# Optimization experiments

Hardware: AMD Instinct MI355X
Metric: run time of the kernel (lower is better)

## Reference

```python
import jax, jax.numpy as jnp
import numpy as np

SKIP = 2 ** -0.5
EPS = 1e-6
DIM = 1024
N_LAYERS = 8
N_HEADS = 16
MAX_SEQ = 1024
B = 4
L = 1024


def get_rot_emb(dim, max_seq_len):
    pos = jnp.arange(max_seq_len, dtype=jnp.float32)
    omega = 1.0 / 10000.0 ** (jnp.arange(0, dim, 2, dtype=jnp.float32) / dim)
    angles = pos[:, None] * omega[None, :]  # [S, dim/2]
    cos = jnp.repeat(jnp.cos(angles), 2, axis=-1)  # [S, dim]
    sin = jnp.repeat(jnp.sin(angles), 2, axis=-1)
    return cos, sin


def setup_inputs() -> dict:
    key = jax.random.key(0)
    ks = jax.random.split(key, 16)
    s = 0.02
    d = DIM
    nl = N_LAYERS
    cos, sin = get_rot_emb(d // N_HEADS, MAX_SEQ)
    inp = {
        'x': jax.random.normal(ks[0], (B, L, d), jnp.float32),
        'c': jax.random.normal(ks[1], (B, 1, d), jnp.float32),
        't': jax.random.normal(ks[2], (B, d), jnp.float32),
        'num_heads': N_HEADS,
        'cos': cos,
        'sin': sin,
        'qkv_w': jax.random.normal(ks[3], (nl, d, 3 * d), jnp.float32) * s,
        'qkv_b': jnp.zeros((nl, 3 * d), jnp.float32),
        'proj_w': jax.random.normal(ks[4], (nl, d, d), jnp.float32) * s,
        'proj_b': jnp.zeros((nl, d), jnp.float32),
        'mlp_w1': jax.random.normal(ks[5], (nl, d, 4 * d), jnp.float32) * s,
        'mlp_b1': jnp.zeros((nl, 4 * d), jnp.float32),
        'mlp_w2': jax.random.normal(ks[6], (nl, 4 * d, d), jnp.float32) * s,
        'mlp_b2': jnp.zeros((nl, d), jnp.float32),
        'adaln_w': jax.random.normal(ks[7], (nl, d, 6 * d), jnp.float32) * s,
        'adaln_b': jnp.zeros((nl, 6 * d), jnp.float32),
    }
    return inp


def layer_norm(x):
    mu = jnp.mean(x, axis=-1, keepdims=True)
    var = jnp.var(x, axis=-1, keepdims=True)
    return (x - mu) * jax.lax.rsqrt(var + EPS)


def rotate_half(q):
    # torch: stack([-q[..., 1::2], q[..., ::2]], -1).reshape(q.shape)
    q2 = q.reshape(q.shape[:-1] + (-1, 2))
    return jnp.stack([-q2[..., 1], q2[..., 0]], axis=-1).reshape(q.shape)


def reference(x, c, t, num_heads, cos, sin, qkv_w, qkv_b, proj_w, proj_b, mlp_w1, mlp_b1, mlp_w2, mlp_b2, adaln_w, adaln_b):
    Bx, Lx, C = x.shape
    H = int(num_heads)
    D = C // H
    scale = D ** -0.5
    cmod = (c + t[:, None]) * SKIP  # [B,1,C]
    cos_l = cos[:Lx]  # [L,D]
    sin_l = sin[:Lx]

    def block(xcur, p):
        qw, qb, pw, pb, w1, b1, w2, b2, aw, ab = p
        mod = jax.nn.silu(cmod) @ aw + ab  # [B,1,6C]
        sh1, sc1, g1, sh2, sc2, g2 = jnp.split(mod, 6, axis=-1)
        h = (layer_norm(xcur) * (1 + sc1) + sh1) * SKIP
        qkv = (h @ qw + qb).reshape(Bx, Lx, 3, H, D).transpose(2, 0, 3, 1, 4)
        q, k, v = qkv[0], qkv[1], qkv[2]  # [B,H,L,D]
        q = q * cos_l + rotate_half(q) * sin_l
        k = k * cos_l + rotate_half(k) * sin_l
        attn = jax.nn.softmax(scale * jnp.einsum('bhid,bhjd->bhij', q, k), axis=-1)
        o = jnp.einsum('bhij,bhjd->bhid', attn, v).transpose(0, 2, 1, 3).reshape(Bx, Lx, C)
        o = o @ pw + pb
        xcur = (xcur + g1 * o) * SKIP
        h2 = (layer_norm(xcur) * (1 + sc2) + sh2) * SKIP
        m = jax.nn.gelu(h2 @ w1 + b1, approximate=True) @ w2 + b2
        return (xcur + g2 * m) * SKIP, None

    params = (qkv_w, qkv_b, proj_w, proj_b, mlp_w1, mlp_b1, mlp_w2, mlp_b2, adaln_w, adaln_b)
    out, _ = jax.lax.scan(block, x, params)
    return out
```

## Files before the change

kernel.cpp:

```cpp
#include <hip/hip_runtime.h>

#define SKIPF 0.70710678118654752440f

typedef unsigned short u16;
typedef unsigned int u32;
typedef __attribute__((ext_vector_type(4))) short bf16x4;
typedef __attribute__((ext_vector_type(8))) short bf16x8;
typedef __attribute__((ext_vector_type(4))) float f32x4;

#define MFMA32(A, B, C) __builtin_amdgcn_mfma_f32_16x16x32_bf16(A, B, C, 0, 0, 0)
#define MFMA16(A, B, C) __builtin_amdgcn_mfma_f32_16x16x16bf16_1k(A, B, C, 0, 0, 0)

__device__ __forceinline__ float bf2f(u16 v) {
  u32 u = ((u32)v) << 16; float f; __builtin_memcpy(&f, &u, 4); return f;
}
__device__ __forceinline__ u16 f2bf(float f) {
  u32 u; __builtin_memcpy(&u, &f, 4);
  u = (u + 0x7fffu + ((u >> 16) & 1u)) >> 16;
  return (u16)u;
}
__device__ __forceinline__ u32 cvtpk(float a, float b) {
  u32 r;
  asm("v_cvt_pk_bf16_f32 %0, %1, %2" : "=v"(r) : "v"(a), "v"(b));
  return r;
}
__device__ __forceinline__ void gload16(const void* g, void* s) {
  __builtin_amdgcn_global_load_lds((const __attribute__((address_space(1))) void*)g,
                                   (__attribute__((address_space(3))) void*)s, 16, 0, 0);
}

__global__ __launch_bounds__(256) void adaln_part_kernel(const float* __restrict__ c,
                                                         const float* __restrict__ t,
                                                         const float* __restrict__ aw,
                                                         float* __restrict__ part) {
  __shared__ float sc[4][32];
  int n = blockIdx.x * 256 + threadIdx.x;
  int ks = blockIdx.y;
  int k0 = ks * 32;
  if (threadIdx.x < 128) {
    int b = threadIdx.x >> 5, kk = threadIdx.x & 31;
    float xx = (c[b * 1024 + k0 + kk] + t[b * 1024 + k0 + kk]) * SKIPF;
    sc[b][kk] = xx / (1.f + __expf(-xx));
  }
  __syncthreads();
  float a0 = 0.f, a1 = 0.f, a2 = 0.f, a3 = 0.f;
#pragma unroll 4
  for (int k = 0; k < 32; ++k) {
    float w = aw[(size_t)(k0 + k) * 6144 + n];
    a0 += sc[0][k] * w; a1 += sc[1][k] * w; a2 += sc[2][k] * w; a3 += sc[3][k] * w;
  }
  part[(size_t)(ks * 4 + 0) * 6144 + n] = a0;
  part[(size_t)(ks * 4 + 1) * 6144 + n] = a1;
  part[(size_t)(ks * 4 + 2) * 6144 + n] = a2;
  part[(size_t)(ks * 4 + 3) * 6144 + n] = a3;
}

__global__ void adaln_reduce_kernel(const float* __restrict__ part, const float* __restrict__ ab,
                                    float* __restrict__ mod) {
  int i = blockIdx.x * 256 + threadIdx.x;
  int b = i / 6144, n = i - b * 6144;
  float a = ab[n];
#pragma unroll 4
  for (int ks = 0; ks < 32; ++ks) a += part[(size_t)(ks * 4 + b) * 6144 + n];
  mod[(size_t)b * 6144 + n] = a;
}

__global__ void wtrans4_kernel(const float* __restrict__ wq, u16* __restrict__ oq,
                               const float* __restrict__ wp, u16* __restrict__ op,
                               const float* __restrict__ w1p, u16* __restrict__ o1,
                               const float* __restrict__ w2p, u16* __restrict__ o2) {
  __shared__ float tile[32][33];
  int bid = blockIdx.x;
  const float* W; u16* WT; int nx, K, N, base;
  if (bid < 3072)      { W = wq;  WT = oq; nx = 96;  K = 1024; N = 3072; base = 0; }
  else if (bid < 4096) { W = wp;  WT = op; nx = 32;  K = 1024; N = 1024; base = 3072; }
  else if (bid < 8192) { W = w1p; WT = o1; nx = 128; K = 1024; N = 4096; base = 4096; }
  else                 { W = w2p; WT = o2; nx = 32;  K = 4096; N = 1024; base = 8192; }
  int t = bid - base;
  int n0 = (t % nx) * 32, k0 = (t / nx) * 32;
  int tx = threadIdx.x, ty = threadIdx.y;
#pragma unroll
  for (int i = 0; i < 4; ++i)
    tile[ty * 4 + i][tx] = W[(size_t)(k0 + ty * 4 + i) * N + n0 + tx];
  __syncthreads();
#pragma unroll
  for (int i = 0; i < 4; ++i)
    WT[(size_t)(n0 + ty * 4 + i) * K + k0 + tx] = f2bf(tile[tx][ty * 4 + i]);
}

__global__ __launch_bounds__(256) void ln_mod_kernel(const float* __restrict__ xin,
                                                     const float* __restrict__ mod,
                                                     u16* __restrict__ h, int sh_off, int sc_off) {
  int row = blockIdx.x;
  int b = row >> 10;
  const float4* xr = (const float4*)(xin + (size_t)row * 1024);
  float4 v = xr[threadIdx.x];
  float s = v.x + v.y + v.z + v.w;
  float ss = v.x * v.x + v.y * v.y + v.z * v.z + v.w * v.w;
#pragma unroll
  for (int o = 32; o; o >>= 1) { s += __shfl_xor(s, o); ss += __shfl_xor(ss, o); }
  __shared__ float red[8];
  int wave = threadIdx.x >> 6;
  if ((threadIdx.x & 63) == 0) { red[wave * 2] = s; red[wave * 2 + 1] = ss; }
  __syncthreads();
  s = red[0] + red[2] + red[4] + red[6];
  ss = red[1] + red[3] + red[5] + red[7];
  float mu = s * (1.f / 1024.f);
  float var = ss * (1.f / 1024.f) - mu * mu;
  float rs = rsqrtf(var + 1e-6f);
  int n = threadIdx.x * 4;
  const float* mb = mod + (size_t)b * 6144;
  float4 sc = *(const float4*)(mb + sc_off + n);
  float4 sh = *(const float4*)(mb + sh_off + n);
  ushort4 o4;
  o4.x = f2bf(((v.x - mu) * rs * (1.f + sc.x) + sh.x) * SKIPF);
  o4.y = f2bf(((v.y - mu) * rs * (1.f + sc.y) + sh.y) * SKIPF);
  o4.z = f2bf(((v.z - mu) * rs * (1.f + sc.z) + sh.z) * SKIPF);
  o4.w = f2bf(((v.w - mu) * rs * (1.f + sc.w) + sh.w) * SKIPF);
  *(ushort4*)(h + (size_t)row * 1024 + n) = o4;
}

template <int EPI>
__global__ __launch_bounds__(512, 1) void gemm256r_kernel(
    const u16* __restrict__ A, const u16* __restrict__ BT, const float* __restrict__ bias,
    u16* __restrict__ Cb, int NBX, int N, int K,
    const float* __restrict__ cosb, const float* __restrict__ sinb,
    u16* __restrict__ qo, u16* __restrict__ ko, u16* __restrict__ vto) {
  __shared__ u16 lds[4][16384];
  const int tid = threadIdx.x;
  const int lane = tid & 63, wave = tid >> 6;
  const int lq = lane & 15, lk = lane >> 4;
  const int wr = wave >> 2, wc = wave & 3;

  int per = gridDim.x >> 3;
  int swz = (blockIdx.x & 7) * per + (blockIdx.x >> 3);
  int bx = swz % NBX, by = swz / NBX;
  const int m0 = by * 256, n0 = bx * 256;

  f32x4 acc[8][4];
#pragma unroll
  for (int i = 0; i < 8; ++i)
#pragma unroll
    for (int j = 0; j < 4; ++j) acc[i][j] = (f32x4){0.f, 0.f, 0.f, 0.f};

  auto STAGE_ONE = [&](int slot, int t, int part) {
    int kt = t * 32;
    int u = tid + (part & 1) * 512;
    int r = u >> 3, cpos = u & 7;
    int g = cpos ^ (r & 7);
    if (part < 2) {
      gload16(A + (size_t)(m0 + 2 * r + (g >> 2)) * K + kt + (g & 3) * 8,
              (char*)lds[slot] + u * 16);
    } else {
      gload16(BT + (size_t)(n0 + 2 * r + (g >> 2)) * K + kt + (g & 3) * 8,
              (char*)(lds[slot] + 8192) + u * 16);
    }
  };
  auto STAGE = [&](int slot, int t) {
#pragma unroll
    for (int p = 0; p < 4; ++p) STAGE_ONE(slot, t, p);
  };

  const int NT = K >> 5;
  STAGE(0, 0); STAGE(1, 1); STAGE(2, 2);
  int slot = 0;
  for (int t = 0; t < NT; ++t) {
    int rem = NT - 1 - t;
    if (rem >= 2) asm volatile("s_waitcnt vmcnt(8)" ::: "memory");
    else if (rem == 1) asm volatile("s_waitcnt vmcnt(4)" ::: "memory");
    else asm volatile("s_waitcnt vmcnt(0)" ::: "memory");
    __builtin_amdgcn_s_barrier();
    __builtin_amdgcn_sched_barrier(0);
    const char* Ab = (const char*)lds[slot];
    const char* Bb = (const char*)(lds[slot] + 8192);
    int ns = slot + 3; if (ns >= 4) ns -= 4;
    bool pre = (t + 3 < NT);
    bf16x8 bfr[4];
#pragma unroll
    for (int ni = 0; ni < 4; ++ni) {
      int nrow = wc * 64 + ni * 16 + lq;
      int r = nrow >> 1, g = (nrow & 1) * 4 + lk;
      bfr[ni] = *(const bf16x8*)(Bb + r * 128 + ((g ^ (r & 7)) << 4));
    }
#pragma unroll
    for (int ph = 0; ph < 4; ++ph) {
      if (pre) STAGE_ONE(ns, t + 3, ph);
      bf16x8 af0, af1;
      {
        int mrow = wr * 128 + (ph * 2) * 16 + lq;
        int r = mrow >> 1, g = (mrow & 1) * 4 + lk;
        af0 = *(const bf16x8*)(Ab + r * 128 + ((g ^ (r & 7)) << 4));
        mrow += 16;
        r = mrow >> 1; g = (mrow & 1) * 4 + lk;
        af1 = *(const bf16x8*)(Ab + r * 128 + ((g ^ (r & 7)) << 4));
      }
      __builtin_amdgcn_s_setprio(1);
#pragma unroll
      for (int j = 0; j < 4; ++j) acc[ph * 2][j] = MFMA32(af0, bfr[j], acc[ph * 2][j]);
#pragma unroll
      for (int j = 0; j < 4; ++j) acc[ph * 2 + 1][j] = MFMA32(af1, bfr[j], acc[ph * 2 + 1][j]);
      __builtin_amdgcn_s_setprio(0);
    }
    ++slot; if (slot >= 4) slot = 0;
  }

#pragma unroll
  for (int i = 0; i < 8; ++i) {
    int rbase = m0 + wr * 128 + i * 16 + lk * 4;
#pragma unroll
    for (int j = 0; j < 4; ++j) {
      int cg = n0 + wc * 64 + j * 16 + lq;
      float bv = bias[cg];
      if (EPI == 2) {
        int region = cg >> 10;
        int cgr = cg & 1023;
        int hh = cgr >> 6, d = cgr & 63;
        int b = rbase >> 10, l0 = rbase & 1023;
        if (region < 2) {
#pragma unroll
          for (int r = 0; r < 4; ++r) {
            int l = l0 + r;
            float val = acc[i][j][r] + bv;
            float partner = __shfl_xor(val, 1);
            float cc = cosb[l * 64 + d], sn = sinb[l * 64 + d];
            float out = (d & 1) ? (val * cc + partner * sn) : (val * cc - partner * sn);
            if (region == 0) out *= 0.125f;
            u16* dst = (region == 0) ? qo : ko;
            dst[((size_t)(b * 16 + hh) * 1024 + l) * 64 + d] = f2bf(out);
          }
        } else {
          union { ushort4 s4; u32 w[2]; } vv;
          vv.w[0] = cvtpk(acc[i][j][0] + bv, acc[i][j][1] + bv);
          vv.w[1] = cvtpk(acc[i][j][2] + bv, acc[i][j][3] + bv);
          *(ushort4*)(vto + (size_t)(b * 16 + hh) * 65536 + (size_t)d * 1024 + l0) = vv.s4;
        }
      } else {
#pragma unroll
        for (int r = 0; r < 4; ++r) {
          int row = rbase + r;
          float val = acc[i][j][r] + bv;
          if (EPI == 0) {
            Cb[(size_t)row * N + cg] = f2bf(val);
          } else {
            float tt = 0.7978845608028654f * (val + 0.044715f * val * val * val);
            float e = __expf(2.f * tt);
            float th = 1.f - 2.f / (e + 1.f);
            Cb[(size_t)row * N + cg] = f2bf(0.5f * val * (1.f + th));
          }
        }
      }
    }
  }
}

__global__ __launch_bounds__(256) void gemm_res128_kernel(
    const u16* __restrict__ A, const u16* __restrict__ BT, const float* __restrict__ bias,
    const float* __restrict__ xin, float* __restrict__ xout, const float* __restrict__ mod,
    int g_off, int K) {
  __shared__ u16 lds[3][8192];
  const int tid = threadIdx.x;
  const int lane = tid & 63, wave = tid >> 6;
  const int lq = lane & 15, lk = lane >> 4;
  const int wr = wave >> 1, wc = wave & 1;
  const int m0 = blockIdx.x * 128, n0 = blockIdx.y * 128;

  f32x4 acc[4][4];
#pragma unroll
  for (int i = 0; i < 4; ++i)
#pragma unroll
    for (int j = 0; j < 4; ++j) acc[i][j] = (f32x4){0.f, 0.f, 0.f, 0.f};

  auto STAGE = [&](int slot, int t) {
    int kt = t * 32;
    char* Ab = (char*)lds[slot];
    char* Bb = (char*)(lds[slot] + 4096);
#pragma unroll
    for (int q = 0; q < 2; ++q) {
      int u = tid + q * 256;
      int r = u >> 3, cpos = u & 7;
      int g = cpos ^ (r & 7);
      gload16(A + (size_t)(m0 + 2 * r + (g >> 2)) * K + kt + (g & 3) * 8, Ab + u * 16);
      gload16(BT + (size_t)(n0 + 2 * r + (g >> 2)) * K + kt + (g & 3) * 8, Bb + u * 16);
    }
  };

  const int NT = K >> 5;
  STAGE(0, 0); STAGE(1, 1);
  int slot = 0;
  for (int t = 0; t < NT; ++t) {
    if (t + 1 < NT) asm volatile("s_waitcnt vmcnt(4)" ::: "memory");
    else asm volatile("s_waitcnt vmcnt(0)" ::: "memory");
    __builtin_amdgcn_s_barrier();
    __builtin_amdgcn_sched_barrier(0);
    if (t + 2 < NT) { int ns = slot + 2; if (ns >= 3) ns -= 3; STAGE(ns, t + 2); }
    const char* Ab = (const char*)lds[slot];
    const char* Bb = (const char*)(lds[slot] + 4096);
    bf16x8 af[4], bfr[4];
#pragma unroll
    for (int i = 0; i < 4; ++i) {
      int mrow = wr * 64 + i * 16 + lq;
      int r = mrow >> 1, g = (mrow & 1) * 4 + lk;
      af[i] = *(const bf16x8*)(Ab + r * 128 + ((g ^ (r & 7)) << 4));
    }
#pragma unroll
    for (int j = 0; j < 4; ++j) {
      int nrow = wc * 64 + j * 16 + lq;
      int r = nrow >> 1, g = (nrow & 1) * 4 + lk;
      bfr[j] = *(const bf16x8*)(Bb + r * 128 + ((g ^ (r & 7)) << 4));
    }
    __builtin_amdgcn_s_setprio(1);
#pragma unroll
    for (int i = 0; i < 4; ++i)
#pragma unroll
      for (int j = 0; j < 4; ++j) acc[i][j] = MFMA32(af[i], bfr[j], acc[i][j]);
    __builtin_amdgcn_s_setprio(0);
    ++slot; if (slot >= 3) slot = 0;
  }

#pragma unroll
  for (int i = 0; i < 4; ++i) {
    int rbase = m0 + wr * 64 + i * 16 + lk * 4;
#pragma unroll
    for (int j = 0; j < 4; ++j) {
      int cg = n0 + wc * 64 + j * 16 + lq;
      float bv = bias[cg];
#pragma unroll
      for (int r = 0; r < 4; ++r) {
        int row = rbase + r;
        float val = acc[i][j][r] + bv;
        int b = row >> 10;
        float g = mod[(size_t)b * 6144 + g_off + cg];
        float xv = xin[(size_t)row * 1024 + cg];
        xout[(size_t)row * 1024 + cg] = (xv + g * val) * SKIPF;
      }
    }
  }
}

__global__ __launch_bounds__(256) void attn_kernel(const u16* __restrict__ qb,
                                                   const u16* __restrict__ kb,
                                                   const u16* __restrict__ vt,
                                                   u16* __restrict__ ob) {
  __shared__ u16 ktile[2][4096];
  __shared__ u16 vtile[2][4096];
  int nid = (blockIdx.x & 7) * 128 + (blockIdx.x >> 3);
  int qt = nid & 15, bh = nid >> 4;
  int tid = threadIdx.x;
  int lane = tid & 63, wave = tid >> 6;
  int lq = lane & 15, lk = lane >> 4;
  const u16* Q = qb + (size_t)bh * 65536;
  const u16* Kp = kb + (size_t)bh * 65536;
  const u16* VT = vt + (size_t)bh * 65536;
  int qbase = qt * 64 + wave * 16;

  bf16x8 qf0 = *(const bf16x8*)(Q + (size_t)(qbase + lq) * 64 + lk * 8);
  bf16x8 qf1 = *(const bf16x8*)(Q + (size_t)(qbase + lq) * 64 + 32 + lk * 8);

  auto stage_one = [&](int buf, int kvb, int u) {
    int r = u >> 3;
    int cc = ((u & 7) ^ (r & 7)) * 8;
    gload16(Kp + (size_t)(kvb + r) * 64 + cc, (char*)ktile[buf] + u * 16);
    gload16(VT + (size_t)r * 1024 + kvb + cc, (char*)vtile[buf] + u * 16);
  };

  float mrun = -1e30f, lsum = 0.f;
  f32x4 oacc[4];
#pragma unroll
  for (int f = 0; f < 4; ++f) oacc[f] = (f32x4){0.f, 0.f, 0.f, 0.f};
  const f32x4 z4 = (f32x4){0.f, 0.f, 0.f, 0.f};

  stage_one(0, 0, tid); stage_one(0, 0, tid + 256);
  int slot = 0;
  for (int t = 0; t < 16; ++t) {
    asm volatile("s_waitcnt vmcnt(0)" ::: "memory");
    __builtin_amdgcn_s_barrier();
    __builtin_amdgcn_sched_barrier(0);
    if (t + 1 < 16) {
      stage_one(slot ^ 1, (t + 1) * 64, tid);
      stage_one(slot ^ 1, (t + 1) * 64, tid + 256);
    }
    const char* kb_ = (const char*)ktile[slot];
    const char* vb_ = (const char*)vtile[slot];
    f32x4 st[4];
    __builtin_amdgcn_s_setprio(1);
#pragma unroll
    for (int s = 0; s < 4; ++s) {
      int r = s * 16 + lq;
      int sw = (r & 7) << 4;
      bf16x8 kf0 = *(const bf16x8*)(kb_ + r * 128 + ((lk * 16) ^ sw));
      bf16x8 kf1 = *(const bf16x8*)(kb_ + r * 128 + ((64 + lk * 16) ^ sw));
      st[s] = MFMA32(kf0, qf0, z4);
      st[s] = MFMA32(kf1, qf1, st[s]);
    }
    __builtin_amdgcn_s_setprio(0);
    float pm = -1e30f;
#pragma unroll
    for (int s = 0; s < 4; ++s)
#pragma unroll
      for (int r = 0; r < 4; ++r) pm = fmaxf(pm, st[s][r]);
    pm = fmaxf(pm, __shfl_xor(pm, 16));
    pm = fmaxf(pm, __shfl_xor(pm, 32));
    if (!__all(pm - mrun <= 8.f)) {
      float mnew = fmaxf(mrun, pm);
      float corr = __expf(mrun - mnew);
      float c0 = __shfl(corr, lk * 4 + 0), c1 = __shfl(corr, lk * 4 + 1);
      float c2 = __shfl(corr, lk * 4 + 2), c3 = __shfl(corr, lk * 4 + 3);
#pragma unroll
      for (int f = 0; f < 4; ++f) {
        oacc[f][0] *= c0; oacc[f][1] *= c1;
        oacc[f][2] *= c2; oacc[f][3] *= c3;
      }
      lsum *= corr;
      mrun = mnew;
    }
    bf16x4 pf[4];
    float ps = 0.f;
#pragma unroll
    for (int s = 0; s < 4; ++s) {
      float p0 = __expf(st[s][0] - mrun);
      float p1 = __expf(st[s][1] - mrun);
      float p2 = __expf(st[s][2] - mrun);
      float p3 = __expf(st[s][3] - mrun);
      ps += p0 + p1 + p2 + p3;
      union { bf16x4 v; u32 w[2]; } pu;
      pu.w[0] = cvtpk(p0, p1);
      pu.w[1] = cvtpk(p2, p3);
      pf[s] = pu.v;
    }
    ps += __shfl_xor(ps, 16);
    ps += __shfl_xor(ps, 32);
    lsum += ps;
    __builtin_amdgcn_s_setprio(1);
#pragma unroll
    for (int f = 0; f < 4; ++f) {
      int r = lq + f * 16;
      int sw = (r & 7) << 4;
#pragma unroll
      for (int s = 0; s < 4; ++s) {
        bf16x4 vf = *(const bf16x4*)(vb_ + r * 128 + ((s * 32 + lk * 8) ^ sw));
        oacc[f] = MFMA16(pf[s], vf, oacc[f]);
      }
    }
    __builtin_amdgcn_s_setprio(0);
    slot ^= 1;
  }

  int b = bh >> 4, hh = bh & 15;
  float inv = 1.f / lsum;
  float i0 = __shfl(inv, lk * 4 + 0), i1 = __shfl(inv, lk * 4 + 1);
  float i2 = __shfl(inv, lk * 4 + 2), i3 = __shfl(inv, lk * 4 + 3);
#pragma unroll
  for (int f = 0; f < 4; ++f) {
#pragma unroll
    for (int j = 0; j < 4; ++j) {
      int qrow = qbase + lk * 4 + j;
      float sc = (j == 0) ? i0 : (j == 1) ? i1 : (j == 2) ? i2 : i3;
      ob[((size_t)(b * 1024 + qrow)) * 1024 + hh * 64 + lq + f * 16] = f2bf(oacc[f][j] * sc);
    }
  }
}


extern "C" void kernel_launch(void* const* d_in, const int* in_sizes, int n_in,
                              void* d_out, int out_size, void* d_ws, size_t ws_size,
                              hipStream_t stream) {
  const float* x = (const float*)d_in[0];
  const float* c = (const float*)d_in[1];
  const float* t = (const float*)d_in[2];
  const float* cosb = (const float*)d_in[4];
  const float* sinb = (const float*)d_in[5];
  const float* qkv_w = (const float*)d_in[6];
  const float* qkv_b = (const float*)d_in[7];
  const float* proj_w = (const float*)d_in[8];
  const float* proj_b = (const float*)d_in[9];
  const float* w1 = (const float*)d_in[10];
  const float* b1 = (const float*)d_in[11];
  const float* w2 = (const float*)d_in[12];
  const float* b2 = (const float*)d_in[13];
  const float* aw = (const float*)d_in[14];
  const float* ab = (const float*)d_in[15];

  constexpr size_t OFF_X = 0;
  constexpr size_t OFF_H = OFF_X + 16777216;
  constexpr size_t OFF_BIG = OFF_H + 8388608;
  constexpr size_t OFF_Q = OFF_BIG + 33554432;
  constexpr size_t OFF_K = OFF_Q + 8388608;
  constexpr size_t OFF_V = OFF_K + 8388608;
  constexpr size_t OFF_AO = OFF_V + 8388608;
  constexpr size_t OFF_WQ = OFF_AO + 8388608;
  constexpr size_t OFF_WP = OFF_WQ + 6291456;
  constexpr size_t OFF_W1 = OFF_WP + 2097152;
  constexpr size_t OFF_W2 = OFF_W1 + 8388608;
  constexpr size_t OFF_MOD = OFF_W2 + 8388608;
  constexpr size_t OFF_PART = OFF_MOD + 98304;

  char* ws = (char*)d_ws;
  float* x_cur = (float*)(ws + OFF_X);
  u16* h = (u16*)(ws + OFF_H);
  u16* big = (u16*)(ws + OFF_BIG);
  u16* qv = (u16*)(ws + OFF_Q);
  u16* kv = (u16*)(ws + OFF_K);
  u16* vt = (u16*)(ws + OFF_V);
  u16* ao = (u16*)(ws + OFF_AO);
  u16* wTq = (u16*)(ws + OFF_WQ);
  u16* wTp = (u16*)(ws + OFF_WP);
  u16* wT1 = (u16*)(ws + OFF_W1);
  u16* wT2 = (u16*)(ws + OFF_W2);
  float* mod = (float*)(ws + OFF_MOD);
  float* part = (float*)(ws + OFF_PART);

  for (int L = 0; L < 8; ++L) {
    const float* awL = aw + (size_t)L * 1024 * 6144;
    const float* abL = ab + (size_t)L * 6144;
    const float* qwL = qkv_w + (size_t)L * 1024 * 3072;
    const float* qbL = qkv_b + (size_t)L * 3072;
    const float* pwL = proj_w + (size_t)L * 1024 * 1024;
    const float* pbL = proj_b + (size_t)L * 1024;
    const float* w1L = w1 + (size_t)L * 1024 * 4096;
    const float* b1L = b1 + (size_t)L * 4096;
    const float* w2L = w2 + (size_t)L * 4096 * 1024;
    const float* b2L = b2 + (size_t)L * 1024;

    const float* xin = (L == 0) ? x : x_cur;
    float* xout2 = (L == 7) ? (float*)d_out : x_cur;

    adaln_part_kernel<<<dim3(24, 32), 256, 0, stream>>>(c, t, awL, part);
    adaln_reduce_kernel<<<96, 256, 0, stream>>>(part, abL, mod);
    wtrans4_kernel<<<12288, dim3(32, 8), 0, stream>>>(qwL, wTq, pwL, wTp, w1L, wT1, w2L, wT2);

    ln_mod_kernel<<<4096, 256, 0, stream>>>(xin, mod, h, 0, 1024);
    gemm256r_kernel<2><<<192, 512, 0, stream>>>(h, wTq, qbL, nullptr, 12, 3072, 1024,
                                                cosb, sinb, qv, kv, vt);
    attn_kernel<<<1024, 256, 0, stream>>>(qv, kv, vt, ao);
    gemm_res128_kernel<<<dim3(32, 8), 256, 0, stream>>>(ao, wTp, pbL, xin, x_cur, mod, 2048, 1024);
    ln_mod_kernel<<<4096, 256, 0, stream>>>(x_cur, mod, h, 3072, 4096);
    gemm256r_kernel<1><<<256, 512, 0, stream>>>(h, wT1, b1L, big, 16, 4096, 1024,
                                                nullptr, nullptr, nullptr, nullptr, nullptr);
    gemm_res128_kernel<<<dim3(32, 8), 256, 0, stream>>>(big, wT2, b2L, x_cur, xout2, mod, 5120, 4096);
  }
}
```

Before: 1.781 ms.

## Deepen residual GEMM pipeline to four stages and interleave loads with MFMAs

The residual-add GEMM kernel moves from a 3-slot to a 4-slot LDS ring, prefetching three K-tiles ahead instead of two, with vmcnt waits adjusted to match. The next-tile global loads are split into four parts and issued between the per-row-group MFMA batches, and A fragments are read from LDS just in time. The aim is to hide global memory latency better and spread VMEM issue across compute. In exchange, LDS use rises to 64KB per block, which may lower occupancy.

Measured after the change: 1.852 ms. 1.04x slower.

```diff
diff --git a/kernel.cpp b/kernel.cpp
--- a/kernel.cpp
+++ b/kernel.cpp
@@ -257,7 +257,7 @@
     const u16* __restrict__ A, const u16* __restrict__ BT, const float* __restrict__ bias,
     const float* __restrict__ xin, float* __restrict__ xout, const float* __restrict__ mod,
     int g_off, int K) {
-  __shared__ u16 lds[3][8192];
+  __shared__ u16 lds[4][8192];
   const int tid = threadIdx.x;
   const int lane = tid & 63, wave = tid >> 6;
   const int lq = lane & 15, lk = lane >> 4;
@@ -270,51 +270,60 @@
 #pragma unroll
     for (int j = 0; j < 4; ++j) acc[i][j] = (f32x4){0.f, 0.f, 0.f, 0.f};
 
+  auto STAGE_ONE = [&](int slot, int t, int part) {
+    int kt = t * 32;
+    int u = tid + (part & 1) * 256;
+    int r = u >> 3, cpos = u & 7;
+    int g = cpos ^ (r & 7);
+    if (part < 2) {
+      gload16(A + (size_t)(m0 + 2 * r + (g >> 2)) * K + kt + (g & 3) * 8,
+              (char*)lds[slot] + u * 16);
+    } else {
+      gload16(BT + (size_t)(n0 + 2 * r + (g >> 2)) * K + kt + (g & 3) * 8,
+              (char*)(lds[slot] + 4096) + u * 16);
+    }
+  };
   auto STAGE = [&](int slot, int t) {
-    int kt = t * 32;
-    char* Ab = (char*)lds[slot];
-    char* Bb = (char*)(lds[slot] + 4096);
-#pragma unroll
-    for (int q = 0; q < 2; ++q) {
-      int u = tid + q * 256;
-      int r = u >> 3, cpos = u & 7;
-      int g = cpos ^ (r & 7);
-      gload16(A + (size_t)(m0 + 2 * r + (g >> 2)) * K + kt + (g & 3) * 8, Ab + u * 16);
-      gload16(BT + (size_t)(n0 + 2 * r + (g >> 2)) * K + kt + (g & 3) * 8, Bb + u * 16);
-    }
+#pragma unroll
+    for (int p = 0; p < 4; ++p) STAGE_ONE(slot, t, p);
   };
 
   const int NT = K >> 5;
-  STAGE(0, 0); STAGE(1, 1);
+  STAGE(0, 0); STAGE(1, 1); STAGE(2, 2);
   int slot = 0;
   for (int t = 0; t < NT; ++t) {
-    if (t + 1 < NT) asm volatile("s_waitcnt vmcnt(4)" ::: "memory");
+    int rem = NT - 1 - t;
+    if (rem >= 2) asm volatile("s_waitcnt vmcnt(8)" ::: "memory");
+    else if (rem == 1) asm volatile("s_waitcnt vmcnt(4)" ::: "memory");
     else asm volatile("s_waitcnt vmcnt(0)" ::: "memory");
     __builtin_amdgcn_s_barrier();
     __builtin_amdgcn_sched_barrier(0);
-    if (t + 2 < NT) { int ns = slot + 2; if (ns >= 3) ns -= 3; STAGE(ns, t + 2); }
     const char* Ab = (const char*)lds[slot];
     const char* Bb = (const char*)(lds[slot] + 4096);
-    bf16x8 af[4], bfr[4];
-#pragma unroll
-    for (int i = 0; i < 4; ++i) {
-      int mrow = wr * 64 + i * 16 + lq;
-      int r = mrow >> 1, g = (mrow & 1) * 4 + lk;
-      af[i] = *(const bf16x8*)(Ab + r * 128 + ((g ^ (r & 7)) << 4));
-    }
+    int ns = slot + 3; if (ns >= 4) ns -= 4;
+    bool pre = (t + 3 < NT);
+    bf16x8 bfr[4];
 #pragma unroll
     for (int j = 0; j < 4; ++j) {
       int nrow = wc * 64 + j * 16 + lq;
       int r = nrow >> 1, g = (nrow & 1) * 4 + lk;
       bfr[j] = *(const bf16x8*)(Bb + r * 128 + ((g ^ (r & 7)) << 4));
     }
-    __builtin_amdgcn_s_setprio(1);
-#pragma unroll
-    for (int i = 0; i < 4; ++i)
-#pragma unroll
-      for (int j = 0; j < 4; ++j) acc[i][j] = MFMA32(af[i], bfr[j], acc[i][j]);
-    __builtin_amdgcn_s_setprio(0);
-    ++slot; if (slot >= 3) slot = 0;
+#pragma unroll
+    for (int i = 0; i < 4; ++i) {
+      if (pre) STAGE_ONE(ns, t + 3, i);
+      bf16x8 af;
+      {
+        int mrow = wr * 64 + i * 16 + lq;
+        int r = mrow >> 1, g = (mrow & 1) * 4 + lk;
+        af = *(const bf16x8*)(Ab + r * 128 + ((g ^ (r & 7)) << 4));
+      }
+      __builtin_amdgcn_s_setprio(1);
+#pragma unroll
+      for (int j = 0; j < 4; ++j) acc[i][j] = MFMA32(af, bfr[j], acc[i][j]);
+      __builtin_amdgcn_s_setprio(0);
+    }
+    ++slot; if (slot >= 4) slot = 0;
   }
 
 #pragma unroll
```
